# Performance work log

Hardware: AMD Instinct MI355X
Metric: run time of the kernel (lower is better)

## Reference

```python
import jax, jax.numpy as jnp
import numpy as np

B, S, E = 16384, 32, 128
H, DH, O = 4, 32, 128  # num_heads, head_dim (qkv_features//num_heads), out_features


def setup_inputs() -> dict:
    key = jax.random.key(0)
    kx, kq, kk, kv, ko = jax.random.split(key, 5)
    return {
        "x": jax.random.normal(kx, (B, S, E), dtype=jnp.float32),
        "w_q": jax.random.normal(kq, (H, E, DH), dtype=jnp.float32),
        "w_k": jax.random.normal(kk, (H, E, DH), dtype=jnp.float32),
        "w_v": jax.random.normal(kv, (H, E, DH), dtype=jnp.float32),
        "w_o": jax.random.normal(ko, (H, DH, O), dtype=jnp.float32),
    }


def reference(x, w_q, w_k, w_v, w_o):
    # Per-head projections: [B, H, S, DH]
    scale = jnp.asarray(w_q.shape[-1] ** -0.5, x.dtype)
    Q = jnp.einsum("bse,hed->bhsd", x, w_q) * scale
    K = jnp.einsum("bse,hed->bhsd", x, w_k)
    V = jnp.einsum("bse,hed->bhsd", x, w_v)
    scores = jnp.einsum("bhsd,bhtd->bhst", Q, K)  # [B, H, S, S]
    A = jax.nn.softmax(scores, axis=-1)
    Hd = jnp.einsum("bhst,bhtd->bhsd", A, V)  # [B, H, S, DH]
    # Per-head output projection, summed across heads: [B, S, O]
    out = jnp.einsum("bhsd,hdo->bso", Hd, w_o)
    return out
```

## Files before the change

### kernel.cpp

```cpp
#include <hip/hip_runtime.h>


typedef __bf16 bf16x8 __attribute__((ext_vector_type(8)));
typedef float f32x4 __attribute__((ext_vector_type(4)));

union FragU { unsigned int w[4]; bf16x8 v; };

__device__ inline unsigned short f2bf(float f) {
  unsigned int u = __builtin_bit_cast(unsigned int, f);
  u += 0x7FFFu + ((u >> 16) & 1u);
  return (unsigned short)(u >> 16);
}
__device__ inline float bf2f(unsigned short h) {
  return __builtin_bit_cast(float, (unsigned int)h << 16);
}

__device__ inline bf16x8 ld_frag8(const unsigned short* p) {
  FragU f;
  const uint2* q = (const uint2*)p;
  uint2 a = q[0], b = q[1];
  f.w[0] = a.x; f.w[1] = a.y; f.w[2] = b.x; f.w[3] = b.y;
  return f.v;
}

__device__ inline f32x4 mfma16(bf16x8 a, bf16x8 b, f32x4 c) {
  return __builtin_amdgcn_mfma_f32_16x16x32_bf16(a, b, c, 0, 0, 0);
}

__device__ inline void copy16(const unsigned short* src, unsigned short* dst) {
  uint4 a = *(const uint4*)src;
  uint4 b = *((const uint4*)src + 1);
  uint2* d = (uint2*)dst;
  d[0] = make_uint2(a.x, a.y); d[1] = make_uint2(a.z, a.w);
  d[2] = make_uint2(b.x, b.y); d[3] = make_uint2(b.z, b.w);
}

__global__ void prep_w(const float* __restrict__ wq, const float* __restrict__ wk,
                       const float* __restrict__ wv, const float* __restrict__ wo,
                       unsigned short* __restrict__ wsb) {
  int idx = blockIdx.x * 256 + threadIdx.x;
  int t = idx >> 14;
  int rem = idx & 16383;
  int hh = rem >> 12;
  int r2 = rem & 4095;
  const float* src = (t == 0) ? wq : (t == 1) ? wk : (t == 2) ? wv : wo;
  float v = src[rem];
  if (t == 0) v *= 0.17677669529663687f;
  int off;
  if (t < 3) { int e = r2 >> 5, d = r2 & 31; off = (hh << 12) + (d << 7) + e; }
  else       { int dh = r2 >> 7, o = r2 & 127; off = (hh << 12) + (o << 5) + dh; }
  unsigned short hi = f2bf(v);
  unsigned short lo = f2bf(v - bf2f(hi));
  wsb[(t << 15) + off] = hi;
  wsb[(t << 15) + 16384 + off] = lo;
}

#define OFF_WB_HI 0
#define OFF_WB_LO 4608
#define OFF_K_HI  9216
#define OFF_K_LO  11520
#define OFF_VT_HI 13824
#define OFF_VT_LO 16128
#define OFF_Q_HI  18432
#define OFF_Q_LO  20736
#define LDS_TOT   23040

__global__ __launch_bounds__(256, 2) void attn_fused(
    const float* __restrict__ x, const unsigned short* __restrict__ wsb,
    float* __restrict__ out) {
  __shared__ unsigned short lds[LDS_TOT];
  const int tid = threadIdx.x;
  const int lane = tid & 63;
  const int wid = tid >> 6;
  const int bl = wid >> 1;
  const int hw = wid & 1;
  const int sbase = hw << 4;
  const int col = lane & 15;
  const int quad = lane >> 4;

  bf16x8 xh[4], xl[4];
  for (int b = 0; b < 2; ++b) {
    const float4* xg = (const float4*)(x + ((long)(blockIdx.x * 2 + b) << 12));
#pragma unroll
    for (int it = 0; it < 4; ++it) {
      int f4 = it * 256 + tid;
      float4 v = xg[f4];
      int s = f4 >> 5;
      int e = (f4 & 31) << 2;
      unsigned short a0 = f2bf(v.x), b0 = f2bf(v.x - bf2f(a0));
      unsigned short a1 = f2bf(v.y), b1 = f2bf(v.y - bf2f(a1));
      unsigned short a2 = f2bf(v.z), b2 = f2bf(v.z - bf2f(a2));
      unsigned short a3 = f2bf(v.w), b3 = f2bf(v.w - bf2f(a3));
      uint2 ph, pl;
      ph.x = (unsigned)a0 | ((unsigned)a1 << 16);
      ph.y = (unsigned)a2 | ((unsigned)a3 << 16);
      pl.x = (unsigned)b0 | ((unsigned)b1 << 16);
      pl.y = (unsigned)b2 | ((unsigned)b3 << 16);
      *(uint2*)(lds + s * 132 + e) = ph;
      *(uint2*)(lds + 4224 + s * 132 + e) = pl;
    }
    __syncthreads();
    if (bl == b) {
#pragma unroll
      for (int kk = 0; kk < 4; ++kk) {
        xh[kk] = ld_frag8(lds + (sbase + col) * 132 + (kk << 5) + (quad << 3));
        xl[kk] = ld_frag8(lds + 4224 + (sbase + col) * 132 + (kk << 5) + (quad << 3));
      }
    }
    __syncthreads();
  }

  const long batch = (long)blockIdx.x * 2 + bl;
  const f32x4 zero = {0.f, 0.f, 0.f, 0.f};
  f32x4 oacc[8];
#pragma unroll
  for (int i = 0; i < 8; ++i) oacc[i] = zero;

  unsigned short* Kh = lds + OFF_K_HI + bl * 1152;
  unsigned short* Kl = lds + OFF_K_LO + bl * 1152;
  unsigned short* Vh = lds + OFF_VT_HI + bl * 1152;
  unsigned short* Vl = lds + OFF_VT_LO + bl * 1152;
  unsigned short* Qh = lds + OFF_Q_HI + (bl * 2 + hw) * 576;
  unsigned short* Ql = lds + OFF_Q_LO + (bl * 2 + hw) * 576;
  unsigned short* Abuf = lds + OFF_K_HI + bl * 1152;

  for (int hh = 0; hh < 4; ++hh) {
    __syncthreads();

    {
      int i0 = tid << 4, d = i0 >> 7, e0 = i0 & 127;
      copy16(wsb + (hh << 12) + i0, lds + OFF_WB_HI + d * 132 + e0);
      copy16(wsb + 16384 + (hh << 12) + i0, lds + OFF_WB_LO + d * 132 + e0);
    }
    __syncthreads();
    f32x4 c0 = zero, c1 = zero;
#pragma unroll
    for (int kk = 0; kk < 4; ++kk) {
      bf16x8 f0 = ld_frag8(lds + OFF_WB_HI + col * 132 + (kk << 5) + (quad << 3));
      bf16x8 f1 = ld_frag8(lds + OFF_WB_HI + (col + 16) * 132 + (kk << 5) + (quad << 3));
      bf16x8 g0 = ld_frag8(lds + OFF_WB_LO + col * 132 + (kk << 5) + (quad << 3));
      bf16x8 g1 = ld_frag8(lds + OFF_WB_LO + (col + 16) * 132 + (kk << 5) + (quad << 3));
      c0 = mfma16(xh[kk], f0, c0); c0 = mfma16(xl[kk], f0, c0); c0 = mfma16(xh[kk], g0, c0);
      c1 = mfma16(xh[kk], f1, c1); c1 = mfma16(xl[kk], f1, c1); c1 = mfma16(xh[kk], g1, c1);
    }
#pragma unroll
    for (int r = 0; r < 4; ++r) {
      int row = (quad << 2) + r;
      unsigned short hi = f2bf(c0[r]), lo = f2bf(c0[r] - bf2f(hi));
      Qh[row * 36 + col] = hi; Ql[row * 36 + col] = lo;
      hi = f2bf(c1[r]); lo = f2bf(c1[r] - bf2f(hi));
      Qh[row * 36 + col + 16] = hi; Ql[row * 36 + col + 16] = lo;
    }
    __syncthreads();

    {
      int i0 = tid << 4, d = i0 >> 7, e0 = i0 & 127;
      copy16(wsb + 32768 + (hh << 12) + i0, lds + OFF_WB_HI + d * 132 + e0);
      copy16(wsb + 32768 + 16384 + (hh << 12) + i0, lds + OFF_WB_LO + d * 132 + e0);
    }
    __syncthreads();
    c0 = zero; c1 = zero;
#pragma unroll
    for (int kk = 0; kk < 4; ++kk) {
      bf16x8 f0 = ld_frag8(lds + OFF_WB_HI + col * 132 + (kk << 5) + (quad << 3));
      bf16x8 f1 = ld_frag8(lds + OFF_WB_HI + (col + 16) * 132 + (kk << 5) + (quad << 3));
      bf16x8 g0 = ld_frag8(lds + OFF_WB_LO + col * 132 + (kk << 5) + (quad << 3));
      bf16x8 g1 = ld_frag8(lds + OFF_WB_LO + (col + 16) * 132 + (kk << 5) + (quad << 3));
      c0 = mfma16(xh[kk], f0, c0); c0 = mfma16(xl[kk], f0, c0); c0 = mfma16(xh[kk], g0, c0);
      c1 = mfma16(xh[kk], f1, c1); c1 = mfma16(xl[kk], f1, c1); c1 = mfma16(xh[kk], g1, c1);
    }
#pragma unroll
    for (int r = 0; r < 4; ++r) {
      int row = sbase + (quad << 2) + r;
      unsigned short hi = f2bf(c0[r]), lo = f2bf(c0[r] - bf2f(hi));
      Kh[row * 36 + col] = hi; Kl[row * 36 + col] = lo;
      hi = f2bf(c1[r]); lo = f2bf(c1[r] - bf2f(hi));
      Kh[row * 36 + col + 16] = hi; Kl[row * 36 + col + 16] = lo;
    }
    __syncthreads();

    {
      int i0 = tid << 4, d = i0 >> 7, e0 = i0 & 127;
      copy16(wsb + 65536 + (hh << 12) + i0, lds + OFF_WB_HI + d * 132 + e0);
      copy16(wsb + 65536 + 16384 + (hh << 12) + i0, lds + OFF_WB_LO + d * 132 + e0);
    }
    __syncthreads();
    c0 = zero; c1 = zero;
#pragma unroll
    for (int kk = 0; kk < 4; ++kk) {
      bf16x8 f0 = ld_frag8(lds + OFF_WB_HI + col * 132 + (kk << 5) + (quad << 3));
      bf16x8 f1 = ld_frag8(lds + OFF_WB_HI + (col + 16) * 132 + (kk << 5) + (quad << 3));
      bf16x8 g0 = ld_frag8(lds + OFF_WB_LO + col * 132 + (kk << 5) + (quad << 3));
      bf16x8 g1 = ld_frag8(lds + OFF_WB_LO + (col + 16) * 132 + (kk << 5) + (quad << 3));
      c0 = mfma16(xh[kk], f0, c0); c0 = mfma16(xl[kk], f0, c0); c0 = mfma16(xh[kk], g0, c0);
      c1 = mfma16(xh[kk], f1, c1); c1 = mfma16(xl[kk], f1, c1); c1 = mfma16(xh[kk], g1, c1);
    }
#pragma unroll
    for (int r = 0; r < 4; ++r) {
      int t = sbase + (quad << 2) + r;
      unsigned short hi = f2bf(c0[r]), lo = f2bf(c0[r] - bf2f(hi));
      Vh[col * 36 + t] = hi; Vl[col * 36 + t] = lo;
      hi = f2bf(c1[r]); lo = f2bf(c1[r] - bf2f(hi));
      Vh[(col + 16) * 36 + t] = hi; Vl[(col + 16) * 36 + t] = lo;
    }
    __syncthreads();

    f32x4 s0 = zero, s1 = zero;
    {
      bf16x8 qhf = ld_frag8(Qh + col * 36 + (quad << 3));
      bf16x8 qlf = ld_frag8(Ql + col * 36 + (quad << 3));
      bf16x8 k0 = ld_frag8(Kh + col * 36 + (quad << 3));
      bf16x8 k1 = ld_frag8(Kh + (col + 16) * 36 + (quad << 3));
      bf16x8 k0l = ld_frag8(Kl + col * 36 + (quad << 3));
      bf16x8 k1l = ld_frag8(Kl + (col + 16) * 36 + (quad << 3));
      s0 = mfma16(qhf, k0, s0); s0 = mfma16(qlf, k0, s0); s0 = mfma16(qhf, k0l, s0);
      s1 = mfma16(qhf, k1, s1); s1 = mfma16(qlf, k1, s1); s1 = mfma16(qhf, k1l, s1);
    }
    float a0[4], a1[4];
#pragma unroll
    for (int r = 0; r < 4; ++r) {
      float v0 = s0[r], v1 = s1[r];
      float mx = fmaxf(v0, v1);
#pragma unroll
      for (int dx = 1; dx < 16; dx <<= 1) mx = fmaxf(mx, __shfl_xor(mx, dx));
      float e0 = __expf(v0 - mx), e1 = __expf(v1 - mx);
      float sm = e0 + e1;
#pragma unroll
      for (int dx = 1; dx < 16; dx <<= 1) sm += __shfl_xor(sm, dx);
      float inv = 1.0f / sm;
      a0[r] = e0 * inv; a1[r] = e1 * inv;
    }
    __syncthreads();
#pragma unroll
    for (int r = 0; r < 4; ++r) {
      int row = sbase + (quad << 2) + r;
      Abuf[row * 36 + col] = f2bf(a0[r]);
      Abuf[row * 36 + col + 16] = f2bf(a1[r]);
    }
    __syncthreads();

    f32x4 hv0 = zero, hv1 = zero;
    {
      bf16x8 af = ld_frag8(Abuf + (sbase + col) * 36 + (quad << 3));
      bf16x8 v0h = ld_frag8(Vh + col * 36 + (quad << 3));
      bf16x8 v1h = ld_frag8(Vh + (col + 16) * 36 + (quad << 3));
      bf16x8 v0l = ld_frag8(Vl + col * 36 + (quad << 3));
      bf16x8 v1l = ld_frag8(Vl + (col + 16) * 36 + (quad << 3));
      hv0 = mfma16(af, v0h, hv0); hv0 = mfma16(af, v0l, hv0);
      hv1 = mfma16(af, v1h, hv1); hv1 = mfma16(af, v1l, hv1);
    }
#pragma unroll
    for (int r = 0; r < 4; ++r) {
      int row = (quad << 2) + r;
      unsigned short hi = f2bf(hv0[r]), lo = f2bf(hv0[r] - bf2f(hi));
      Qh[row * 36 + col] = hi; Ql[row * 36 + col] = lo;
      hi = f2bf(hv1[r]); lo = f2bf(hv1[r] - bf2f(hi));
      Qh[row * 36 + col + 16] = hi; Ql[row * 36 + col + 16] = lo;
    }
    {
      int i0 = tid << 4, o = i0 >> 5, d0 = i0 & 31;
      copy16(wsb + 98304 + (hh << 12) + i0, lds + OFF_WB_HI + o * 36 + d0);
      copy16(wsb + 98304 + 16384 + (hh << 12) + i0, lds + OFF_WB_LO + o * 36 + d0);
    }
    __syncthreads();
    {
      bf16x8 dh = ld_frag8(Qh + col * 36 + (quad << 3));
      bf16x8 dl = ld_frag8(Ql + col * 36 + (quad << 3));
#pragma unroll
      for (int t8 = 0; t8 < 8; ++t8) {
        bf16x8 wh = ld_frag8(lds + OFF_WB_HI + ((t8 << 4) + col) * 36 + (quad << 3));
        bf16x8 wl = ld_frag8(lds + OFF_WB_LO + ((t8 << 4) + col) * 36 + (quad << 3));
        oacc[t8] = mfma16(dh, wh, oacc[t8]);
        oacc[t8] = mfma16(dl, wh, oacc[t8]);
        oacc[t8] = mfma16(dh, wl, oacc[t8]);
      }
    }
  }

  float* og = out + batch * 4096;
#pragma unroll
  for (int t8 = 0; t8 < 8; ++t8) {
#pragma unroll
    for (int r = 0; r < 4; ++r) {
      og[(sbase + (quad << 2) + r) * 128 + (t8 << 4) + col] = oacc[t8][r];
    }
  }
}

extern "C" void kernel_launch(void* const* d_in, const int* in_sizes, int n_in,
                              void* d_out, int out_size, void* d_ws, size_t ws_size,
                              hipStream_t stream) {
  const float* x = (const float*)d_in[0];
  const float* wq = (const float*)d_in[1];
  const float* wk = (const float*)d_in[2];
  const float* wv = (const float*)d_in[3];
  const float* wo = (const float*)d_in[4];
  float* out = (float*)d_out;
  unsigned short* wsb = (unsigned short*)d_ws;
  hipLaunchKernelGGL(prep_w, dim3(256), dim3(256), 0, stream, wq, wk, wv, wo, wsb);
  hipLaunchKernelGGL(attn_fused, dim3(8192), dim3(256), 0, stream, x, wsb, out);
}
```

Before: 707.9 us.

## Stage weights via direct global-to-LDS loads with XOR swizzle and fewer barriers

Changes the prep kernel to write the split hi/lo bf16 weights in an XOR-swizzled, per-head contiguous layout. The fused kernel then stages each weight slice with global_load_lds straight into LDS, skipping register round trips, and reads it back with 16-byte conflict-free fragment loads. Each weight load now overlaps with the previous projection's Q/K/V writeback, and some barriers are removed or replaced with lighter waitcnt plus s_barrier macros. Also adds a dedicated attention buffer, hardware bf16 conversion, s_setprio around MFMA bursts, and raises the launch-bounds occupancy hint to 3 blocks per CU. The added LDS and the reduced barriers risk occupancy limits or race conditions if the sync placement is wrong.

```diff
diff --git a/kernel.cpp b/kernel.cpp
--- a/kernel.cpp
+++ b/kernel.cpp
@@ -2,14 +2,13 @@
 
 
 typedef __bf16 bf16x8 __attribute__((ext_vector_type(8)));
+typedef __bf16 bf16x2 __attribute__((ext_vector_type(2)));
 typedef float f32x4 __attribute__((ext_vector_type(4)));
 
 union FragU { unsigned int w[4]; bf16x8 v; };
 
 __device__ inline unsigned short f2bf(float f) {
-  unsigned int u = __builtin_bit_cast(unsigned int, f);
-  u += 0x7FFFu + ((u >> 16) & 1u);
-  return (unsigned short)(u >> 16);
+  return __builtin_bit_cast(unsigned short, (__bf16)f);
 }
 __device__ inline float bf2f(unsigned short h) {
   return __builtin_bit_cast(float, (unsigned int)h << 16);
@@ -22,17 +21,57 @@
   f.w[0] = a.x; f.w[1] = a.y; f.w[2] = b.x; f.w[3] = b.y;
   return f.v;
 }
+__device__ inline bf16x8 ld_frag16(const unsigned short* p) {
+  FragU f;
+  uint4 a = *(const uint4*)p;
+  f.w[0] = a.x; f.w[1] = a.y; f.w[2] = a.z; f.w[3] = a.w;
+  return f.v;
+}
 
 __device__ inline f32x4 mfma16(bf16x8 a, bf16x8 b, f32x4 c) {
   return __builtin_amdgcn_mfma_f32_16x16x32_bf16(a, b, c, 0, 0, 0);
 }
 
-__device__ inline void copy16(const unsigned short* src, unsigned short* dst) {
-  uint4 a = *(const uint4*)src;
-  uint4 b = *((const uint4*)src + 1);
-  uint2* d = (uint2*)dst;
-  d[0] = make_uint2(a.x, a.y); d[1] = make_uint2(a.z, a.w);
-  d[2] = make_uint2(b.x, b.y); d[3] = make_uint2(b.z, b.w);
+__device__ inline void wb_pair(unsigned short* dhi, unsigned short* dlo, float v) {
+  __bf16 h = (__bf16)v;
+  *dhi = __builtin_bit_cast(unsigned short, h);
+  *dlo = f2bf(v - (float)h);
+}
+
+#define SYNC_LDS() do { asm volatile("s_waitcnt lgkmcnt(0)" ::: "memory"); \
+                        __builtin_amdgcn_s_barrier(); \
+                        asm volatile("" ::: "memory"); } while (0)
+#define SYNC_VM()  do { asm volatile("s_waitcnt vmcnt(0) lgkmcnt(0)" ::: "memory"); \
+                        __builtin_amdgcn_s_barrier(); \
+                        asm volatile("" ::: "memory"); } while (0)
+
+__device__ inline void stage4(const unsigned short* wt, unsigned short* ldsb,
+                              int widu, int lane) {
+  const char* g = (const char*)wt + (widu << 12) + (lane << 4);
+  char* l = (char*)ldsb + (widu << 12);
+#pragma unroll
+  for (int j = 0; j < 4; ++j) {
+    __builtin_amdgcn_global_load_lds(
+        (const __attribute__((address_space(1))) void*)(g + (j << 10)),
+        (__attribute__((address_space(3))) void*)(l + (j << 10)),
+        16, 0, 0);
+  }
+}
+
+__device__ inline void proj3(const unsigned short* lds, int col, int quad,
+                             const bf16x8* xh, const bf16x8* xl,
+                             f32x4& c0, f32x4& c1) {
+#pragma unroll
+  for (int kk = 0; kk < 4; ++kk) {
+    int swz = ((((kk << 2) | quad) ^ col) << 3);
+    const unsigned short* ph = lds + (col << 7) + swz;
+    bf16x8 f0 = ld_frag16(ph);
+    bf16x8 f1 = ld_frag16(ph + 2048);
+    bf16x8 g0 = ld_frag16(ph + 4096);
+    bf16x8 g1 = ld_frag16(ph + 6144);
+    c0 = mfma16(xh[kk], f0, c0); c0 = mfma16(xl[kk], f0, c0); c0 = mfma16(xh[kk], g0, c0);
+    c1 = mfma16(xh[kk], f1, c1); c1 = mfma16(xl[kk], f1, c1); c1 = mfma16(xh[kk], g1, c1);
+  }
 }
 
 __global__ void prep_w(const float* __restrict__ wq, const float* __restrict__ wk,
@@ -46,32 +85,39 @@
   const float* src = (t == 0) ? wq : (t == 1) ? wk : (t == 2) ? wv : wo;
   float v = src[rem];
   if (t == 0) v *= 0.17677669529663687f;
-  int off;
-  if (t < 3) { int e = r2 >> 5, d = r2 & 31; off = (hh << 12) + (d << 7) + e; }
-  else       { int dh = r2 >> 7, o = r2 & 127; off = (hh << 12) + (o << 5) + dh; }
-  unsigned short hi = f2bf(v);
-  unsigned short lo = f2bf(v - bf2f(hi));
-  wsb[(t << 15) + off] = hi;
-  wsb[(t << 15) + 16384 + off] = lo;
+  int phys;
+  if (t < 3) {
+    int e = r2 >> 5, d = r2 & 31;
+    phys = (d << 7) + (((e >> 3) ^ (d & 15)) << 3) + (e & 7);
+  } else {
+    int dh = r2 >> 7, o = r2 & 127;
+    phys = (o << 5) + (((dh >> 3) ^ ((o >> 1) & 3)) << 3) + (dh & 7);
+  }
+  int base = ((t << 2) | hh) << 13;
+  __bf16 h = (__bf16)v;
+  wsb[base + phys] = __builtin_bit_cast(unsigned short, h);
+  wsb[base + 4096 + phys] = f2bf(v - (float)h);
 }
 
 #define OFF_WB_HI 0
-#define OFF_WB_LO 4608
-#define OFF_K_HI  9216
-#define OFF_K_LO  11520
-#define OFF_VT_HI 13824
-#define OFF_VT_LO 16128
-#define OFF_Q_HI  18432
-#define OFF_Q_LO  20736
-#define LDS_TOT   23040
-
-__global__ __launch_bounds__(256, 2) void attn_fused(
+#define OFF_WB_LO 4096
+#define OFF_A     8192
+#define OFF_K_HI  10496
+#define OFF_K_LO  12800
+#define OFF_VT_HI 15104
+#define OFF_VT_LO 17408
+#define OFF_Q_HI  19712
+#define OFF_Q_LO  22016
+#define LDS_TOT   24320
+
+__global__ __launch_bounds__(256, 3) void attn_fused(
     const float* __restrict__ x, const unsigned short* __restrict__ wsb,
     float* __restrict__ out) {
-  __shared__ unsigned short lds[LDS_TOT];
+  __shared__ __align__(16) unsigned short lds[LDS_TOT];
   const int tid = threadIdx.x;
   const int lane = tid & 63;
   const int wid = tid >> 6;
+  const int widu = __builtin_amdgcn_readfirstlane(wid);
   const int bl = wid >> 1;
   const int hw = wid & 1;
   const int sbase = hw << 4;
@@ -87,15 +133,12 @@
       float4 v = xg[f4];
       int s = f4 >> 5;
       int e = (f4 & 31) << 2;
-      unsigned short a0 = f2bf(v.x), b0 = f2bf(v.x - bf2f(a0));
-      unsigned short a1 = f2bf(v.y), b1 = f2bf(v.y - bf2f(a1));
-      unsigned short a2 = f2bf(v.z), b2 = f2bf(v.z - bf2f(a2));
-      unsigned short a3 = f2bf(v.w), b3 = f2bf(v.w - bf2f(a3));
-      uint2 ph, pl;
-      ph.x = (unsigned)a0 | ((unsigned)a1 << 16);
-      ph.y = (unsigned)a2 | ((unsigned)a3 << 16);
-      pl.x = (unsigned)b0 | ((unsigned)b1 << 16);
-      pl.y = (unsigned)b2 | ((unsigned)b3 << 16);
+      __bf16 h0 = (__bf16)v.x, h1 = (__bf16)v.y, h2 = (__bf16)v.z, h3 = (__bf16)v.w;
+      bf16x2 hp0 = {h0, h1}, hp1 = {h2, h3};
+      bf16x2 lp0 = {(__bf16)(v.x - (float)h0), (__bf16)(v.y - (float)h1)};
+      bf16x2 lp1 = {(__bf16)(v.z - (float)h2), (__bf16)(v.w - (float)h3)};
+      uint2 ph = {__builtin_bit_cast(unsigned int, hp0), __builtin_bit_cast(unsigned int, hp1)};
+      uint2 pl = {__builtin_bit_cast(unsigned int, lp0), __builtin_bit_cast(unsigned int, lp1)};
       *(uint2*)(lds + s * 132 + e) = ph;
       *(uint2*)(lds + 4224 + s * 132 + e) = pl;
     }
@@ -122,88 +165,56 @@
   unsigned short* Vl = lds + OFF_VT_LO + bl * 1152;
   unsigned short* Qh = lds + OFF_Q_HI + (bl * 2 + hw) * 576;
   unsigned short* Ql = lds + OFF_Q_LO + (bl * 2 + hw) * 576;
-  unsigned short* Abuf = lds + OFF_K_HI + bl * 1152;
+  unsigned short* Abuf = lds + OFF_A + bl * 1152;
 
   for (int hh = 0; hh < 4; ++hh) {
-    __syncthreads();
-
-    {
-      int i0 = tid << 4, d = i0 >> 7, e0 = i0 & 127;
-      copy16(wsb + (hh << 12) + i0, lds + OFF_WB_HI + d * 132 + e0);
-      copy16(wsb + 16384 + (hh << 12) + i0, lds + OFF_WB_LO + d * 132 + e0);
-    }
-    __syncthreads();
+    SYNC_LDS();
+    stage4(wsb + (hh << 13), lds, widu, lane);
+    SYNC_VM();
+
     f32x4 c0 = zero, c1 = zero;
-#pragma unroll
-    for (int kk = 0; kk < 4; ++kk) {
-      bf16x8 f0 = ld_frag8(lds + OFF_WB_HI + col * 132 + (kk << 5) + (quad << 3));
-      bf16x8 f1 = ld_frag8(lds + OFF_WB_HI + (col + 16) * 132 + (kk << 5) + (quad << 3));
-      bf16x8 g0 = ld_frag8(lds + OFF_WB_LO + col * 132 + (kk << 5) + (quad << 3));
-      bf16x8 g1 = ld_frag8(lds + OFF_WB_LO + (col + 16) * 132 + (kk << 5) + (quad << 3));
-      c0 = mfma16(xh[kk], f0, c0); c0 = mfma16(xl[kk], f0, c0); c0 = mfma16(xh[kk], g0, c0);
-      c1 = mfma16(xh[kk], f1, c1); c1 = mfma16(xl[kk], f1, c1); c1 = mfma16(xh[kk], g1, c1);
-    }
+    __builtin_amdgcn_s_setprio(1);
+    proj3(lds, col, quad, xh, xl, c0, c1);
+    __builtin_amdgcn_s_setprio(0);
+
+    SYNC_LDS();
+    stage4(wsb + ((4 + hh) << 13), lds, widu, lane);
 #pragma unroll
     for (int r = 0; r < 4; ++r) {
       int row = (quad << 2) + r;
-      unsigned short hi = f2bf(c0[r]), lo = f2bf(c0[r] - bf2f(hi));
-      Qh[row * 36 + col] = hi; Ql[row * 36 + col] = lo;
-      hi = f2bf(c1[r]); lo = f2bf(c1[r] - bf2f(hi));
-      Qh[row * 36 + col + 16] = hi; Ql[row * 36 + col + 16] = lo;
-    }
-    __syncthreads();
-
-    {
-      int i0 = tid << 4, d = i0 >> 7, e0 = i0 & 127;
-      copy16(wsb + 32768 + (hh << 12) + i0, lds + OFF_WB_HI + d * 132 + e0);
-      copy16(wsb + 32768 + 16384 + (hh << 12) + i0, lds + OFF_WB_LO + d * 132 + e0);
-    }
-    __syncthreads();
+      wb_pair(Qh + row * 36 + col, Ql + row * 36 + col, c0[r]);
+      wb_pair(Qh + row * 36 + col + 16, Ql + row * 36 + col + 16, c1[r]);
+    }
+    SYNC_VM();
+
     c0 = zero; c1 = zero;
-#pragma unroll
-    for (int kk = 0; kk < 4; ++kk) {
-      bf16x8 f0 = ld_frag8(lds + OFF_WB_HI + col * 132 + (kk << 5) + (quad << 3));
-      bf16x8 f1 = ld_frag8(lds + OFF_WB_HI + (col + 16) * 132 + (kk << 5) + (quad << 3));
-      bf16x8 g0 = ld_frag8(lds + OFF_WB_LO + col * 132 + (kk << 5) + (quad << 3));
-      bf16x8 g1 = ld_frag8(lds + OFF_WB_LO + (col + 16) * 132 + (kk << 5) + (quad << 3));
-      c0 = mfma16(xh[kk], f0, c0); c0 = mfma16(xl[kk], f0, c0); c0 = mfma16(xh[kk], g0, c0);
-      c1 = mfma16(xh[kk], f1, c1); c1 = mfma16(xl[kk], f1, c1); c1 = mfma16(xh[kk], g1, c1);
-    }
+    __builtin_amdgcn_s_setprio(1);
+    proj3(lds, col, quad, xh, xl, c0, c1);
+    __builtin_amdgcn_s_setprio(0);
+
+    SYNC_LDS();
+    stage4(wsb + ((8 + hh) << 13), lds, widu, lane);
 #pragma unroll
     for (int r = 0; r < 4; ++r) {
       int row = sbase + (quad << 2) + r;
-      unsigned short hi = f2bf(c0[r]), lo = f2bf(c0[r] - bf2f(hi));
-      Kh[row * 36 + col] = hi; Kl[row * 36 + col] = lo;
-      hi = f2bf(c1[r]); lo = f2bf(c1[r] - bf2f(hi));
-      Kh[row * 36 + col + 16] = hi; Kl[row * 36 + col + 16] = lo;
-    }
-    __syncthreads();
-
-    {
-      int i0 = tid << 4, d = i0 >> 7, e0 = i0 & 127;
-      copy16(wsb + 65536 + (hh << 12) + i0, lds + OFF_WB_HI + d * 132 + e0);
-      copy16(wsb + 65536 + 16384 + (hh << 12) + i0, lds + OFF_WB_LO + d * 132 + e0);
-    }
-    __syncthreads();
+      wb_pair(Kh + row * 36 + col, Kl + row * 36 + col, c0[r]);
+      wb_pair(Kh + row * 36 + col + 16, Kl + row * 36 + col + 16, c1[r]);
+    }
+    SYNC_VM();
+
     c0 = zero; c1 = zero;
-#pragma unroll
-    for (int kk = 0; kk < 4; ++kk) {
-      bf16x8 f0 = ld_frag8(lds + OFF_WB_HI + col * 132 + (kk << 5) + (quad << 3));
-      bf16x8 f1 = ld_frag8(lds + OFF_WB_HI + (col + 16) * 132 + (kk << 5) + (quad << 3));
-      bf16x8 g0 = ld_frag8(lds + OFF_WB_LO + col * 132 + (kk << 5) + (quad << 3));
-      bf16x8 g1 = ld_frag8(lds + OFF_WB_LO + (col + 16) * 132 + (kk << 5) + (quad << 3));
-      c0 = mfma16(xh[kk], f0, c0); c0 = mfma16(xl[kk], f0, c0); c0 = mfma16(xh[kk], g0, c0);
-      c1 = mfma16(xh[kk], f1, c1); c1 = mfma16(xl[kk], f1, c1); c1 = mfma16(xh[kk], g1, c1);
-    }
+    __builtin_amdgcn_s_setprio(1);
+    proj3(lds, col, quad, xh, xl, c0, c1);
+    __builtin_amdgcn_s_setprio(0);
+
+    SYNC_LDS();
+    stage4(wsb + ((12 + hh) << 13), lds, widu, lane);
 #pragma unroll
     for (int r = 0; r < 4; ++r) {
       int t = sbase + (quad << 2) + r;
-      unsigned short hi = f2bf(c0[r]), lo = f2bf(c0[r] - bf2f(hi));
-      Vh[col * 36 + t] = hi; Vl[col * 36 + t] = lo;
-      hi = f2bf(c1[r]); lo = f2bf(c1[r] - bf2f(hi));
-      Vh[(col + 16) * 36 + t] = hi; Vl[(col + 16) * 36 + t] = lo;
-    }
-    __syncthreads();
+      wb_pair(Vh + col * 36 + t, Vl + col * 36 + t, c0[r]);
+      wb_pair(Vh + (col + 16) * 36 + t, Vl + (col + 16) * 36 + t, c1[r]);
+    }
 
     f32x4 s0 = zero, s1 = zero;
     {
@@ -230,14 +241,13 @@
       float inv = 1.0f / sm;
       a0[r] = e0 * inv; a1[r] = e1 * inv;
     }
-    __syncthreads();
 #pragma unroll
     for (int r = 0; r < 4; ++r) {
       int row = sbase + (quad << 2) + r;
       Abuf[row * 36 + col] = f2bf(a0[r]);
       Abuf[row * 36 + col + 16] = f2bf(a1[r]);
     }
-    __syncthreads();
+    SYNC_VM();
 
     f32x4 hv0 = zero, hv1 = zero;
     {
@@ -252,28 +262,24 @@
 #pragma unroll
     for (int r = 0; r < 4; ++r) {
       int row = (quad << 2) + r;
-      unsigned short hi = f2bf(hv0[r]), lo = f2bf(hv0[r] - bf2f(hi));
-      Qh[row * 36 + col] = hi; Ql[row * 36 + col] = lo;
-      hi = f2bf(hv1[r]); lo = f2bf(hv1[r] - bf2f(hi));
-      Qh[row * 36 + col + 16] = hi; Ql[row * 36 + col + 16] = lo;
-    }
-    {
-      int i0 = tid << 4, o = i0 >> 5, d0 = i0 & 31;
-      copy16(wsb + 98304 + (hh << 12) + i0, lds + OFF_WB_HI + o * 36 + d0);
-      copy16(wsb + 98304 + 16384 + (hh << 12) + i0, lds + OFF_WB_LO + o * 36 + d0);
-    }
-    __syncthreads();
+      wb_pair(Qh + row * 36 + col, Ql + row * 36 + col, hv0[r]);
+      wb_pair(Qh + row * 36 + col + 16, Ql + row * 36 + col + 16, hv1[r]);
+    }
     {
       bf16x8 dh = ld_frag8(Qh + col * 36 + (quad << 3));
       bf16x8 dl = ld_frag8(Ql + col * 36 + (quad << 3));
+      int swzo = (quad ^ ((col >> 1) & 3)) << 3;
+      __builtin_amdgcn_s_setprio(1);
 #pragma unroll
       for (int t8 = 0; t8 < 8; ++t8) {
-        bf16x8 wh = ld_frag8(lds + OFF_WB_HI + ((t8 << 4) + col) * 36 + (quad << 3));
-        bf16x8 wl = ld_frag8(lds + OFF_WB_LO + ((t8 << 4) + col) * 36 + (quad << 3));
+        const unsigned short* wp = lds + (((t8 << 4) + col) << 5) + swzo;
+        bf16x8 wh = ld_frag16(wp);
+        bf16x8 wl = ld_frag16(wp + 4096);
         oacc[t8] = mfma16(dh, wh, oacc[t8]);
         oacc[t8] = mfma16(dl, wh, oacc[t8]);
         oacc[t8] = mfma16(dh, wl, oacc[t8]);
       }
+      __builtin_amdgcn_s_setprio(0);
     }
   }
 
```

Measured after the change: 635.1 us. 1.11x faster.
